# Performance work log

Measured on AMD Instinct MI355X. Metric: run time of the kernel, lower is better.

Reference implementation:

```python
import jax, jax.numpy as jnp
import numpy as np

VOCAB, EMBED_DIM, ENCODE_DIM = 50000, 128, 128
B, N = 512, 500            # trees per batch, nodes per tree
MAX_DEPTH = 40             # static bound on tree depth (uniform-attachment trees stay far below)


def setup_inputs() -> dict:
    rng = np.random.default_rng(0)
    T = B * N
    tokens = rng.integers(0, VOCAB, size=T).astype(np.int64)
    # random recursive trees: node i attaches to a uniformly random earlier node
    u = rng.random((B, N))
    pl = np.floor(u * np.arange(N)).astype(np.int64)  # local parent; node 0 is root
    depth = np.zeros((B, N), dtype=np.int64)
    rows = np.arange(B)
    for i in range(1, N):
        depth[:, i] = depth[rows, pl[:, i]] + 1
    assert depth.max() < MAX_DEPTH
    parent = pl + (np.arange(B)[:, None] * N)
    parent[:, 0] = T  # roots scatter into a dummy row
    node2batch = np.repeat(np.arange(B), N).astype(np.int64)

    key = jax.random.key(0)
    k1, k2, k3 = jax.random.split(key, 3)
    emb = jax.random.normal(k1, (VOCAB, EMBED_DIM), jnp.float32) * 0.02
    Wc = jax.random.normal(k2, (EMBED_DIM, ENCODE_DIM), jnp.float32) * 0.05
    bc = jax.random.normal(k3, (ENCODE_DIM,), jnp.float32) * 0.01
    return {
        "tokens": jnp.asarray(tokens),
        "parent": jnp.asarray(parent.reshape(-1)),
        "depth": jnp.asarray(depth.reshape(-1)),
        "node2batch": jnp.asarray(node2batch),
        "emb": emb, "Wc": Wc, "bc": bc, "bs": B,
    }


def reference(tokens, parent, depth, node2batch, emb, Wc, bc, bs):
    T = tokens.shape[0]
    # per-node W_c(embedding(token))  [T, D]
    x = emb[tokens] @ Wc + bc
    # bottom-up subtree sums: v(n) = sum_{m in subtree(n)} x[m]
    v = jnp.concatenate([x, jnp.zeros((1, x.shape[1]), x.dtype)], axis=0)  # +1 dummy row
    for d in range(MAX_DEPTH, 0, -1):
        contrib = jnp.where((depth == d)[:, None], v[:T], jnp.zeros((), x.dtype))
        v = v.at[parent].add(contrib)  # depth-d nodes push into depth d-1 parents
    node_vals = v[:T]
    # per-tree elementwise max over node values (node_list max-pool)
    out = jax.ops.segment_max(node_vals, node2batch, num_segments=bs)
    # rows absent from a node_list entry are zero, so the pool includes 0
    return jnp.maximum(out, jnp.zeros((), out.dtype))
```

## Files before the change

kernel.cpp:

```cpp
#include <hip/hip_runtime.h>
#include <hip/hip_bf16.h>

#define B_BATCH 512
#define NPB     500
#define DIM     128
#define VOCAB   50000
#define MAXD    40
#define NPREP   512
#define NGEMM   ((VOCAB + 63) / 64)

typedef short bf16x8 __attribute__((ext_vector_type(8)));
typedef float f32x4  __attribute__((ext_vector_type(4)));

__device__ __forceinline__ unsigned short f2bf(float x) {
    unsigned u = __float_as_uint(x);
    return (unsigned short)((u + 0x7fffu + ((u >> 16) & 1u)) >> 16);
}

__global__ __launch_bounds__(256) void prep_gemm(const int* __restrict__ tokens,
                                                 const int* __restrict__ parent,
                                                 const int* __restrict__ depth,
                                                 const float* __restrict__ emb,
                                                 const float* __restrict__ Wc,
                                                 const float* __restrict__ bc,
                                                 int* __restrict__ tokD,
                                                 unsigned short* __restrict__ endD,
                                                 unsigned short* __restrict__ Eb) {
    const int tid = threadIdx.x;

    if (blockIdx.x >= NPREP) {
        const int lane = tid & 63, w = tid >> 6;
        const int q = lane >> 4, mc = lane & 15;
        const int rowBase = (blockIdx.x - NPREP) * 64;
        const int arow = min(rowBase + w * 16 + mc, VOCAB - 1);

        f32x4 acc[8];
        #pragma unroll
        for (int nt = 0; nt < 8; ++nt) acc[nt] = (f32x4){0.f, 0.f, 0.f, 0.f};

        #pragma unroll
        for (int kc = 0; kc < 4; ++kc) {
            const float* src = &emb[(long long)arow * DIM + kc * 32 + q * 8];
            float4 v0 = *(const float4*)src;
            float4 v1 = *(const float4*)(src + 4);
            unsigned short aw[8] = {f2bf(v0.x), f2bf(v0.y), f2bf(v0.z), f2bf(v0.w),
                                    f2bf(v1.x), f2bf(v1.y), f2bf(v1.z), f2bf(v1.w)};
            bf16x8 a = *(bf16x8*)aw;
            #pragma unroll
            for (int nt = 0; nt < 8; ++nt) {
                unsigned short bw[8];
                #pragma unroll
                for (int j = 0; j < 8; ++j)
                    bw[j] = f2bf(Wc[(kc * 32 + q * 8 + j) * DIM + nt * 16 + mc]);
                bf16x8 bfr = *(bf16x8*)bw;
                acc[nt] = __builtin_amdgcn_mfma_f32_16x16x32_bf16(a, bfr, acc[nt], 0, 0, 0);
            }
        }

        #pragma unroll
        for (int nt = 0; nt < 8; ++nt) {
            float bcv = bc[nt * 16 + mc];
            #pragma unroll
            for (int r = 0; r < 4; ++r) {
                int grow = rowBase + w * 16 + q * 4 + r;
                if (grow < VOCAB)
                    Eb[(long long)grow * DIM + nt * 16 + mc] = f2bf(acc[nt][r] + bcv);
            }
        }
        return;
    }

    __shared__ unsigned short parL[NPB];
    __shared__ unsigned short depL[NPB];
    __shared__ int   tokL[NPB];
    __shared__ int   sizeL[NPB];
    __shared__ int   pack[NPB];
    __shared__ unsigned short sibp[NPB];
    __shared__ unsigned short tinL[NPB];
    __shared__ unsigned short bucket[NPB];
    __shared__ int hist[MAXD + 1], off[MAXD + 1], cur[MAXD + 1];
    __shared__ int tmpTok[NPB];
    __shared__ unsigned short tmpEnd[NPB];
    __shared__ int sdmax;

    const int b = blockIdx.x;
    const long long base = (long long)b * NPB;

    if (tid <= MAXD) hist[tid] = 0;
    __syncthreads();
    for (int n = tid; n < NPB; n += 256) {
        int d = depth[base + n];
        depL[n]  = (unsigned short)d;
        parL[n]  = (unsigned short)(n == 0 ? 0 : (int)(parent[base + n] - base));
        tokL[n]  = tokens[base + n];
        sizeL[n] = 1;
        if (n > 0) atomicAdd(&hist[d], 1);
    }
    __syncthreads();

    if (tid < 64) {
        int h = (tid >= 1 && tid <= MAXD) ? hist[tid] : 0;
        int x = h;
        #pragma unroll
        for (int o = 1; o < 64; o <<= 1) { int y = __shfl_up(x, o, 64); if (tid >= o) x += y; }
        if (tid >= 1 && tid <= MAXD) { off[tid] = x - h; cur[tid] = x - h; }
        int dm = (h > 0) ? tid : 0;
        #pragma unroll
        for (int o = 32; o; o >>= 1) dm = max(dm, __shfl_down(dm, o));
        if (tid == 0) sdmax = dm;
    }
    __syncthreads();

    for (int n = 1 + tid; n < NPB; n += 256)
        bucket[atomicAdd(&cur[depL[n]], 1)] = (unsigned short)n;
    __syncthreads();
    const int dmax = sdmax;

    for (int d = dmax; d >= 1; --d) {
        int c = hist[d], o = off[d];
        for (int i = tid; i < c; i += 256) {
            int n = bucket[o + i];
            atomicAdd(&sizeL[parL[n]], sizeL[n]);
        }
        __syncthreads();
    }

    for (int n = tid; n < NPB; n += 256) pack[n] = (int)parL[n] | (sizeL[n] << 16);
    __syncthreads();

    {
        int n0 = tid, n1 = tid + 256;
        int p0 = parL[n0];
        int p1 = (n1 < NPB) ? parL[n1] : -1;
        int a0 = 0, a1 = 0;
        for (int m = 1; m < NPB; ++m) {
            int pk = pack[m];
            int pm = pk & 0xffff, sm = pk >> 16;
            if (m < n0 && pm == p0) a0 += sm;
            if (m < n1 && pm == p1) a1 += sm;
        }
        if (n0 >= 1) sibp[n0] = (unsigned short)a0;
        if (n1 >= 1 && n1 < NPB) sibp[n1] = (unsigned short)a1;
        if (tid == 0) tinL[0] = 0;
    }
    __syncthreads();

    for (int d = 1; d <= dmax; ++d) {
        int c = hist[d], o = off[d];
        for (int i = tid; i < c; i += 256) {
            int n = bucket[o + i];
            tinL[n] = (unsigned short)((int)tinL[parL[n]] + 1 + (int)sibp[n]);
        }
        __syncthreads();
    }

    for (int n = tid; n < NPB; n += 256) {
        int t = tinL[n];
        tmpTok[t] = tokL[n];
        tmpEnd[t] = (unsigned short)(t + sizeL[n] - 1);
    }
    __syncthreads();
    for (int t = tid; t < NPB; t += 256) {
        tokD[base + t] = tmpTok[t];
        endD[base + t] = tmpEnd[t];
    }
}

__global__ __launch_bounds__(512, 4) void scan_k(const int* __restrict__ tokD,
                                                 const unsigned short* __restrict__ endD,
                                                 const unsigned short* __restrict__ Eb,
                                                 float* __restrict__ out) {
    const int b = blockIdx.x & 511, s = blockIdx.x >> 9, tid = threadIdx.x;
    const long long base = (long long)b * NPB;
    __shared__ unsigned short Sbf[NPB * 32];
    __shared__ unsigned short endL[NPB];
    __shared__ float partials[16 * 32];
    __shared__ float wmax[8 * 32];

    #pragma unroll
    for (int u = 0; u < 4; ++u) {
        int n = (tid >> 2) + u * 128;
        if (n < NPB) {
            int tok = tokD[base + n];
            const unsigned short* g = &Eb[(long long)tok * DIM + s * 32 + (tid & 3) * 8];
            __builtin_amdgcn_global_load_lds(
                (const __attribute__((address_space(1))) void*)g,
                (__attribute__((address_space(3))) void*)&Sbf[n * 32 + (tid & 3) * 8],
                16, 0, 0);
        }
    }
    if (tid < NPB) endL[tid] = endD[base + tid];
    __syncthreads();

    const int j = tid & 31, c = tid >> 5;
    float x[32];
    {
        float run = 0.f;
        #pragma unroll
        for (int k = 0; k < 32; ++k) {
            int t = c * 32 + k;
            float v = (t < NPB)
                ? __uint_as_float((unsigned)Sbf[t * 32 + j] << 16) : 0.f;
            run += v; x[k] = run;
        }
        partials[c * 32 + j] = run;
    }
    __syncthreads();
    float off = 0.f;
    for (int cc = 0; cc < c; ++cc) off += partials[cc * 32 + j];
    #pragma unroll
    for (int k = 0; k < 32; ++k) {
        int t = c * 32 + k;
        x[k] += off;
        if (t < NPB) Sbf[t * 32 + j] = f2bf(x[k]);
    }
    __syncthreads();

    float m = -INFINITY;
    #pragma unroll
    for (int k = 0; k < 32; ++k) {
        int t = c * 32 + k;
        if (t < NPB) {
            float hi = __uint_as_float((unsigned)Sbf[(int)endL[t] * 32 + j] << 16);
            float lo = (k > 0) ? x[k - 1] : off;
            m = fmaxf(m, hi - lo);
        }
    }
    m = fmaxf(m, __shfl_down(m, 32));
    if ((tid & 63) < 32) wmax[(tid >> 6) * 32 + j] = m;
    __syncthreads();
    if (tid < 32) {
        float mm = wmax[tid];
        #pragma unroll
        for (int w = 1; w < 8; ++w) mm = fmaxf(mm, wmax[w * 32 + tid]);
        out[b * DIM + s * 32 + tid] = fmaxf(mm, 0.0f);
    }
}

extern "C" void kernel_launch(void* const* d_in, const int* in_sizes, int n_in,
                              void* d_out, int out_size, void* d_ws, size_t ws_size,
                              hipStream_t stream) {
    const int*   tokens = (const int*)d_in[0];
    const int*   parent = (const int*)d_in[1];
    const int*   depth  = (const int*)d_in[2];
    const float* emb    = (const float*)d_in[4];
    const float* Wc     = (const float*)d_in[5];
    const float* bc     = (const float*)d_in[6];
    float*       out    = (float*)d_out;

    unsigned short* Eb   = (unsigned short*)d_ws;
    int*            tokD = (int*)(Eb + (long long)VOCAB * DIM);
    unsigned short* endD = (unsigned short*)(tokD + B_BATCH * NPB);

    prep_gemm<<<NPREP + NGEMM, 256, 0, stream>>>(tokens, parent, depth,
                                                 emb, Wc, bc, tokD, endD, Eb);
    scan_k<<<B_BATCH * 4, 512, 0, stream>>>(tokD, endD, Eb, out);
}
```

Before: 145.4 us.

## Stage Wc tile in LDS for GEMM and compute sibling offsets via atomics

The GEMM blocks now load each 32-row slice of Wc with coalesced float4 reads, convert it to bf16 and store it transposed in shared memory, so the MFMA B fragments come from LDS instead of strided scalar global loads with repeated conversions. The prep blocks replace the O(N^2) scan over all nodes that computed sibling prefix sizes with a single atomicAdd per node into a per-parent cursor. The atomic version assigns sibling offsets in nondeterministic order, so the preorder layout differs from run to run, although subtree ranges stay valid. The GEMM path adds two barriers per k-chunk.

```diff
diff --git a/kernel.cpp b/kernel.cpp
--- a/kernel.cpp
+++ b/kernel.cpp
@@ -29,6 +29,8 @@
     const int tid = threadIdx.x;
 
     if (blockIdx.x >= NPREP) {
+        __shared__ __align__(16) unsigned short WcT[DIM * 32];
+
         const int lane = tid & 63, w = tid >> 6;
         const int q = lane >> 4, mc = lane & 15;
         const int rowBase = (blockIdx.x - NPREP) * 64;
@@ -38,21 +40,33 @@
         #pragma unroll
         for (int nt = 0; nt < 8; ++nt) acc[nt] = (f32x4){0.f, 0.f, 0.f, 0.f};
 
+        const int kk = tid >> 3;
+        const int c0 = (tid & 7) * 16;
+
         #pragma unroll
         for (int kc = 0; kc < 4; ++kc) {
+            const float* wsrc = &Wc[(kc * 32 + kk) * DIM + c0];
+            float wv[16];
+            *(float4*)(wv + 0)  = *(const float4*)(wsrc + 0);
+            *(float4*)(wv + 4)  = *(const float4*)(wsrc + 4);
+            *(float4*)(wv + 8)  = *(const float4*)(wsrc + 8);
+            *(float4*)(wv + 12) = *(const float4*)(wsrc + 12);
+            __syncthreads();
+            #pragma unroll
+            for (int i = 0; i < 16; ++i)
+                WcT[(c0 + i) * 32 + kk] = f2bf(wv[i]);
+            __syncthreads();
+
             const float* src = &emb[(long long)arow * DIM + kc * 32 + q * 8];
             float4 v0 = *(const float4*)src;
             float4 v1 = *(const float4*)(src + 4);
             unsigned short aw[8] = {f2bf(v0.x), f2bf(v0.y), f2bf(v0.z), f2bf(v0.w),
                                     f2bf(v1.x), f2bf(v1.y), f2bf(v1.z), f2bf(v1.w)};
             bf16x8 a = *(bf16x8*)aw;
+
             #pragma unroll
             for (int nt = 0; nt < 8; ++nt) {
-                unsigned short bw[8];
-                #pragma unroll
-                for (int j = 0; j < 8; ++j)
-                    bw[j] = f2bf(Wc[(kc * 32 + q * 8 + j) * DIM + nt * 16 + mc]);
-                bf16x8 bfr = *(bf16x8*)bw;
+                bf16x8 bfr = *(bf16x8*)&WcT[(nt * 16 + mc) * 32 + q * 8];
                 acc[nt] = __builtin_amdgcn_mfma_f32_16x16x32_bf16(a, bfr, acc[nt], 0, 0, 0);
             }
         }
@@ -74,7 +88,7 @@
     __shared__ unsigned short depL[NPB];
     __shared__ int   tokL[NPB];
     __shared__ int   sizeL[NPB];
-    __shared__ int   pack[NPB];
+    __shared__ int   childCur[NPB];
     __shared__ unsigned short sibp[NPB];
     __shared__ unsigned short tinL[NPB];
     __shared__ unsigned short bucket[NPB];
@@ -94,6 +108,7 @@
         parL[n]  = (unsigned short)(n == 0 ? 0 : (int)(parent[base + n] - base));
         tokL[n]  = tokens[base + n];
         sizeL[n] = 1;
+        childCur[n] = 0;
         if (n > 0) atomicAdd(&hist[d], 1);
     }
     __syncthreads();
@@ -125,24 +140,9 @@
         __syncthreads();
     }
 
-    for (int n = tid; n < NPB; n += 256) pack[n] = (int)parL[n] | (sizeL[n] << 16);
-    __syncthreads();
-
-    {
-        int n0 = tid, n1 = tid + 256;
-        int p0 = parL[n0];
-        int p1 = (n1 < NPB) ? parL[n1] : -1;
-        int a0 = 0, a1 = 0;
-        for (int m = 1; m < NPB; ++m) {
-            int pk = pack[m];
-            int pm = pk & 0xffff, sm = pk >> 16;
-            if (m < n0 && pm == p0) a0 += sm;
-            if (m < n1 && pm == p1) a1 += sm;
-        }
-        if (n0 >= 1) sibp[n0] = (unsigned short)a0;
-        if (n1 >= 1 && n1 < NPB) sibp[n1] = (unsigned short)a1;
-        if (tid == 0) tinL[0] = 0;
-    }
+    for (int n = 1 + tid; n < NPB; n += 256)
+        sibp[n] = (unsigned short)atomicAdd(&childCur[parL[n]], sizeL[n]);
+    if (tid == 0) tinL[0] = 0;
     __syncthreads();
 
     for (int d = 1; d <= dmax; ++d) {
```

Result: faster. 131.3 us (-9.7%).
